# Kernel tuning notes

Hardware: AMD Instinct MI355X
Metric: run time of the kernel (lower is better)

Reference implementation:

```python
import jax, jax.numpy as jnp
import numpy as np

HEADS = 2
NEG_SLOPE = 0.2  # PyG GATConv default leaky_relu slope


def gat_conv(x, edge_index, W, a_src, a_dst, bias, num_nodes):
    """PyG-style GATConv with concat=True and self-loops.
    x: [N, Fin], W: [Fin, H*C], a_src/a_dst: [H, C], bias: [H*C].
    edge_index: [2, E] with row 0 = source j, row 1 = target i.
    """
    H = HEADS
    C = W.shape[1] // H
    # add self loops
    loops = jnp.arange(num_nodes, dtype=edge_index.dtype)
    src = jnp.concatenate([edge_index[0], loops])
    dst = jnp.concatenate([edge_index[1], loops])

    xW = (x @ W).reshape(num_nodes, H, C)            # [N, H, C]
    alpha_s = jnp.einsum('nhc,hc->nh', xW, a_src)    # [N, H]
    alpha_d = jnp.einsum('nhc,hc->nh', xW, a_dst)    # [N, H]
    e = alpha_s[src] + alpha_d[dst]                  # [E, H]
    e = jax.nn.leaky_relu(e, NEG_SLOPE)
    # segment softmax over edges sharing the same target node
    m = jax.ops.segment_max(e, dst, num_segments=num_nodes)  # [N, H]
    e = jnp.exp(e - m[dst])
    denom = jax.ops.segment_sum(e, dst, num_segments=num_nodes)  # [N, H]
    alpha = e / denom[dst]                           # [E, H]
    # message = alpha_ij * xW_j, aggregated at target i
    msg = xW[src] * alpha[:, :, None]                # [E, H, C]
    out = jax.ops.segment_sum(msg, dst, num_segments=num_nodes)  # [N, H, C]
    return out.reshape(num_nodes, H * C) + bias


def setup_inputs() -> dict:
    key = jax.random.key(0)
    ks = jax.random.split(key, 10)
    N, E = 50000, 800000
    Fin, D = 128, 128
    H = HEADS
    x = jax.random.normal(ks[0], (N, Fin), dtype=jnp.float32)
    edge_index = jax.random.randint(ks[1], (2, E), 0, N, dtype=jnp.int64)
    g = 1.0 / np.sqrt(Fin)
    W1 = jax.random.normal(ks[2], (Fin, H * D), dtype=jnp.float32) * g
    a_src1 = jax.random.normal(ks[3], (H, D), dtype=jnp.float32) * g
    a_dst1 = jax.random.normal(ks[4], (H, D), dtype=jnp.float32) * g
    b1 = jnp.zeros((H * D,), dtype=jnp.float32)
    g2 = 1.0 / np.sqrt(H * D)
    W2 = jax.random.normal(ks[5], (H * D, H * D), dtype=jnp.float32) * g2
    a_src2 = jax.random.normal(ks[6], (H, D), dtype=jnp.float32) * g2
    a_dst2 = jax.random.normal(ks[7], (H, D), dtype=jnp.float32) * g2
    b2 = jnp.zeros((H * D,), dtype=jnp.float32)
    return {"x": x, "edge_index": edge_index,
            "W1": W1, "a_src1": a_src1, "a_dst1": a_dst1, "b1": b1,
            "W2": W2, "a_src2": a_src2, "a_dst2": a_dst2, "b2": b2}


def reference(x, edge_index, W1, a_src1, a_dst1, b1, W2, a_src2, a_dst2, b2):
    N = x.shape[0]
    h = gat_conv(x, edge_index, W1, a_src1, a_dst1, b1, N)
    h = jax.nn.elu(h)
    # dropout is identity in eval mode (deterministic reference)
    out = gat_conv(h, edge_index, W2, a_src2, a_dst2, b2, N)
    return out
```

## Files before the change

### kernel.cpp

```cpp
#include <hip/hip_runtime.h>
#include <math.h>

#define HEADS 2
#define CH    128
#define HC    256
#define NEG   0.2f

typedef __attribute__((ext_vector_type(8))) short  bfrag8;
typedef __attribute__((ext_vector_type(4))) float  f32x4;

__device__ inline unsigned short f2bf_rne(float x) {
    unsigned u = __float_as_uint(x);
    u += 0x7fffu + ((u >> 16) & 1u);
    return (unsigned short)(u >> 16);
}

__global__ __launch_bounds__(256)
void wcast_kernel(const float* __restrict__ W, unsigned short* __restrict__ Wt, int K) {
    const int idx = blockIdx.x * 256 + threadIdx.x;
    if (idx >= K * HC) return;
    const int k = idx >> 8;
    const int n = idx & 255;
    Wt[(size_t)n * K + k] = f2bf_rne(W[idx]);
}

__global__ __launch_bounds__(256)
void va_kernel(const float* __restrict__ W, const float* __restrict__ a_src,
               const float* __restrict__ a_dst, float* __restrict__ va, int K) {
    const int k    = (blockIdx.x * 256 + threadIdx.x) >> 6;
    const int lane = threadIdx.x & 63;
    if (k >= K) return;
    const int c0 = lane * 4;
    const float4 w4 = *reinterpret_cast<const float4*>(&W[(size_t)k * HC + c0]);
    const float4 s4 = *reinterpret_cast<const float4*>(&a_src[c0]);
    const float4 d4 = *reinterpret_cast<const float4*>(&a_dst[c0]);
    float ps = w4.x * s4.x + w4.y * s4.y + w4.z * s4.z + w4.w * s4.w;
    float pd = w4.x * d4.x + w4.y * d4.y + w4.z * d4.z + w4.w * d4.w;
    #pragma unroll
    for (int m = 1; m <= 16; m <<= 1) {
        ps += __shfl_xor(ps, m);
        pd += __shfl_xor(pd, m);
    }
    if (lane == 0)  { va[k * 4 + 0] = ps; va[k * 4 + 2] = pd; }
    if (lane == 32) { va[k * 4 + 1] = ps; va[k * 4 + 3] = pd; }
}

__global__ __launch_bounds__(256)
void xprep_kernel(const float* __restrict__ x, const float* __restrict__ va,
                  unsigned short* __restrict__ xb, float* __restrict__ as_out,
                  float* __restrict__ ad_out, int N, int K) {
    const int i    = (blockIdx.x * 256 + threadIdx.x) >> 6;
    const int lane = threadIdx.x & 63;
    if (i >= N) return;
    const float2 v = reinterpret_cast<const float2*>(&x[(size_t)i * K])[lane];
    ushort2 bv; bv.x = f2bf_rne(v.x); bv.y = f2bf_rne(v.y);
    reinterpret_cast<ushort2*>(&xb[(size_t)i * K])[lane] = bv;

    const float4 a0 = reinterpret_cast<const float4*>(va)[lane * 2 + 0];
    const float4 a1 = reinterpret_cast<const float4*>(va)[lane * 2 + 1];
    float p0 = v.x * a0.x + v.y * a1.x;
    float p1 = v.x * a0.y + v.y * a1.y;
    float p2 = v.x * a0.z + v.y * a1.z;
    float p3 = v.x * a0.w + v.y * a1.w;
    #pragma unroll
    for (int m = 1; m <= 32; m <<= 1) {
        p0 += __shfl_xor(p0, m);
        p1 += __shfl_xor(p1, m);
        p2 += __shfl_xor(p2, m);
        p3 += __shfl_xor(p3, m);
    }
    if (lane == 0) {
        as_out[i * 2 + 0] = p0; as_out[i * 2 + 1] = p1;
        ad_out[i * 2 + 0] = p2; ad_out[i * 2 + 1] = p3;
    }
}

__global__ __launch_bounds__(256)
void gemm_msg_kernel(const unsigned short* __restrict__ Ab,
                     const unsigned short* __restrict__ Wt,
                     unsigned short* __restrict__ xWb, int M, int K) {
    __shared__ unsigned short Ah[128][40];
    __shared__ unsigned short Bh[128][40];

    const int t    = threadIdx.x;
    const int row0 = blockIdx.x * 128;
    const int col0 = blockIdx.y * 128;
    const int lane = t & 63;
    const int wid  = t >> 6;
    const int wr   = wid >> 1;
    const int wc   = wid & 1;

    f32x4 acc[4][4] = {};

    const int arow = t & 127;
    const int aseg = (t >> 7) * 16;

    for (int kk = 0; kk < K; kk += 32) {
        {
            const int gr = row0 + arow;
            bfrag8 v0 = {0,0,0,0,0,0,0,0}, v1 = {0,0,0,0,0,0,0,0};
            if (gr < M) {
                v0 = *reinterpret_cast<const bfrag8*>(&Ab[(size_t)gr * K + kk + aseg]);
                v1 = *reinterpret_cast<const bfrag8*>(&Ab[(size_t)gr * K + kk + aseg + 8]);
            }
            *reinterpret_cast<bfrag8*>(&Ah[arow][aseg])     = v0;
            *reinterpret_cast<bfrag8*>(&Ah[arow][aseg + 8]) = v1;
            const bfrag8 w0 = *reinterpret_cast<const bfrag8*>(
                &Wt[(size_t)(col0 + arow) * K + kk + aseg]);
            const bfrag8 w1 = *reinterpret_cast<const bfrag8*>(
                &Wt[(size_t)(col0 + arow) * K + kk + aseg + 8]);
            *reinterpret_cast<bfrag8*>(&Bh[arow][aseg])     = w0;
            *reinterpret_cast<bfrag8*>(&Bh[arow][aseg + 8]) = w1;
        }
        __syncthreads();

        bfrag8 ah[4], bh[4];
        const int ko = (lane >> 4) * 8;
        #pragma unroll
        for (int m = 0; m < 4; ++m)
            ah[m] = *reinterpret_cast<const bfrag8*>(&Ah[wr * 64 + m * 16 + (lane & 15)][ko]);
        #pragma unroll
        for (int n = 0; n < 4; ++n)
            bh[n] = *reinterpret_cast<const bfrag8*>(&Bh[wc * 64 + n * 16 + (lane & 15)][ko]);

        #pragma unroll
        for (int m = 0; m < 4; ++m)
            #pragma unroll
            for (int n = 0; n < 4; ++n)
                acc[m][n] = __builtin_amdgcn_mfma_f32_16x16x32_bf16(ah[m], bh[n], acc[m][n], 0, 0, 0);
        __syncthreads();
    }

    #pragma unroll
    for (int m = 0; m < 4; ++m) {
        #pragma unroll
        for (int reg = 0; reg < 4; ++reg) {
            const int gr = row0 + wr * 64 + m * 16 + (lane >> 4) * 4 + reg;
            if (gr < M) {
                unsigned short* rp = &xWb[(size_t)gr * HC + col0];
                #pragma unroll
                for (int n = 0; n < 4; ++n)
                    rp[wc * 64 + n * 16 + (lane & 15)] = f2bf_rne(acc[m][n][reg]);
            }
        }
    }
}

__global__ __launch_bounds__(256)
void hist_kernel(const int* __restrict__ dst, int* __restrict__ counts, int E) {
    const int e = blockIdx.x * 256 + threadIdx.x;
    if (e < E) atomicAdd(&counts[dst[e]], 1);
}

__global__ __launch_bounds__(256)
void scan_local_kernel(int* __restrict__ data, int* __restrict__ chunk_sum, int N) {
    __shared__ int s[256];
    const int t   = threadIdx.x;
    const int idx = blockIdx.x * 256 + t;
    const int v   = (idx < N) ? data[idx] : 0;
    s[t] = v;
    __syncthreads();
    #pragma unroll
    for (int off = 1; off < 256; off <<= 1) {
        int x = (t >= off) ? s[t - off] : 0;
        __syncthreads();
        s[t] += x;
        __syncthreads();
    }
    if (idx < N) data[idx] = s[t] - v;
    if (t == 255) chunk_sum[blockIdx.x] = s[255];
}

__global__ __launch_bounds__(256)
void scan_chunks_kernel(int* __restrict__ chunk, int nb) {
    __shared__ int s[256];
    const int t = threadIdx.x;
    const int v = (t < nb) ? chunk[t] : 0;
    s[t] = v;
    __syncthreads();
    #pragma unroll
    for (int off = 1; off < 256; off <<= 1) {
        int x = (t >= off) ? s[t - off] : 0;
        __syncthreads();
        s[t] += x;
        __syncthreads();
    }
    if (t < nb) chunk[t] = s[t] - v;
}

__global__ __launch_bounds__(256)
void add_offsets_kernel(const int* __restrict__ excl, const int* __restrict__ chunk_excl,
                        int* __restrict__ row_ptr, int* __restrict__ cursor,
                        int N, int E) {
    const int idx = blockIdx.x * 256 + threadIdx.x;
    if (idx < N) {
        const int rp = excl[idx] + chunk_excl[idx >> 8];
        row_ptr[idx] = rp;
        cursor[idx]  = rp;
    }
    if (idx == 0) row_ptr[N] = E;
}

__global__ __launch_bounds__(256)
void scatter_kernel(const int* __restrict__ src, const int* __restrict__ dst,
                    int* __restrict__ cursor, int* __restrict__ col_idx, int E) {
    const int e = blockIdx.x * 256 + threadIdx.x;
    if (e < E) {
        const int pos = atomicAdd(&cursor[dst[e]], 1);
        col_idx[pos] = src[e];
    }
}

__global__ __launch_bounds__(256)
void agg_kernel(const int* __restrict__ row_ptr, const int* __restrict__ col_idx,
                const unsigned short* __restrict__ xWb,
                const float* __restrict__ as_, const float* __restrict__ ad_,
                const float* __restrict__ bias, float* __restrict__ outf,
                unsigned short* __restrict__ hb, const float* __restrict__ va,
                float* __restrict__ as2, float* __restrict__ ad2,
                int N, int mode) {
    const int wv   = (blockIdx.x * 256 + threadIdx.x) >> 6;
    const int lane = threadIdx.x & 63;
    if (wv >= N) return;
    const int i    = wv;
    const int half = lane >> 5;
    const int sl   = lane & 31;
    const int hh   = sl >> 4;
    const int cb   = hh * 128 + (sl & 15) * 8;
    const float adi = ad_[i * 2 + hh];

    float acc[8] = {};
    float dn = 0.f;

    const int beg = row_ptr[i];
    const int end = row_ptr[i + 1];

    int k = beg + half;
    int j = (k < end) ? col_idx[k] : 0;
    float asj = as_[j * 2 + hh];
    for (; k < end; k += 2) {
        const int kn = k + 2;
        const int jn = (kn < end) ? col_idx[kn] : 0;
        const float asn = as_[jn * 2 + hh];
        float e = asj + adi;
        e = e > 0.f ? e : NEG * e;
        const float w = expf(e);
        const uint4 q = *reinterpret_cast<const uint4*>(&xWb[(size_t)j * HC + cb]);
        const unsigned qq[4] = {q.x, q.y, q.z, q.w};
        #pragma unroll
        for (int r = 0; r < 4; ++r) {
            const float flo = __uint_as_float(qq[r] << 16);
            const float fhi = __uint_as_float(qq[r] & 0xffff0000u);
            acc[r * 2 + 0] = fmaf(w, flo, acc[r * 2 + 0]);
            acc[r * 2 + 1] = fmaf(w, fhi, acc[r * 2 + 1]);
        }
        dn += w;
        j = jn; asj = asn;
    }

    #pragma unroll
    for (int r = 0; r < 8; ++r) acc[r] += __shfl_xor(acc[r], 32);
    dn += __shfl_xor(dn, 32);

    if (lane < 32) {
        float e = as_[i * 2 + hh] + adi;
        e = e > 0.f ? e : NEG * e;
        const float ws = expf(e);
        const uint4 q = *reinterpret_cast<const uint4*>(&xWb[(size_t)i * HC + cb]);
        const unsigned qq[4] = {q.x, q.y, q.z, q.w};
        #pragma unroll
        for (int r = 0; r < 4; ++r) {
            const float flo = __uint_as_float(qq[r] << 16);
            const float fhi = __uint_as_float(qq[r] & 0xffff0000u);
            acc[r * 2 + 0] = fmaf(ws, flo, acc[r * 2 + 0]);
            acc[r * 2 + 1] = fmaf(ws, fhi, acc[r * 2 + 1]);
        }
        dn += ws;

        const float inv = 1.f / dn;
        const float4 b0 = *reinterpret_cast<const float4*>(&bias[cb]);
        const float4 b1 = *reinterpret_cast<const float4*>(&bias[cb + 4]);
        float o[8];
        o[0] = acc[0] * inv + b0.x; o[1] = acc[1] * inv + b0.y;
        o[2] = acc[2] * inv + b0.z; o[3] = acc[3] * inv + b0.w;
        o[4] = acc[4] * inv + b1.x; o[5] = acc[5] * inv + b1.y;
        o[6] = acc[6] * inv + b1.z; o[7] = acc[7] * inv + b1.w;

        if (mode) {
            #pragma unroll
            for (int r = 0; r < 8; ++r) o[r] = o[r] > 0.f ? o[r] : expm1f(o[r]);
            bfrag8 hv;
            #pragma unroll
            for (int r = 0; r < 8; ++r) hv[r] = (short)f2bf_rne(o[r]);
            *reinterpret_cast<bfrag8*>(&hb[(size_t)i * HC + cb]) = hv;
            float p0 = 0.f, p1 = 0.f, p2 = 0.f, p3 = 0.f;
            #pragma unroll
            for (int r = 0; r < 8; ++r) {
                const float4 vv = reinterpret_cast<const float4*>(va)[cb + r];
                p0 = fmaf(o[r], vv.x, p0);
                p1 = fmaf(o[r], vv.y, p1);
                p2 = fmaf(o[r], vv.z, p2);
                p3 = fmaf(o[r], vv.w, p3);
            }
            #pragma unroll
            for (int m = 1; m <= 16; m <<= 1) {
                p0 += __shfl_xor(p0, m);
                p1 += __shfl_xor(p1, m);
                p2 += __shfl_xor(p2, m);
                p3 += __shfl_xor(p3, m);
            }
            if (sl == 0) {
                as2[i * 2 + 0] = p0; as2[i * 2 + 1] = p1;
                ad2[i * 2 + 0] = p2; ad2[i * 2 + 1] = p3;
            }
        } else {
            *reinterpret_cast<float4*>(&outf[(size_t)i * HC + cb]) =
                make_float4(o[0], o[1], o[2], o[3]);
            *reinterpret_cast<float4*>(&outf[(size_t)i * HC + cb + 4]) =
                make_float4(o[4], o[5], o[6], o[7]);
        }
    }
}

extern "C" void kernel_launch(void* const* d_in, const int* in_sizes, int n_in,
                              void* d_out, int out_size, void* d_ws, size_t ws_size,
                              hipStream_t stream) {
    const float* x      = (const float*)d_in[0];
    const int*   ei     = (const int*)d_in[1];
    const float* W1     = (const float*)d_in[2];
    const float* a_src1 = (const float*)d_in[3];
    const float* a_dst1 = (const float*)d_in[4];
    const float* b1     = (const float*)d_in[5];
    const float* W2     = (const float*)d_in[6];
    const float* a_src2 = (const float*)d_in[7];
    const float* a_dst2 = (const float*)d_in[8];
    const float* b2     = (const float*)d_in[9];
    float* out = (float*)d_out;

    const int Nn = in_sizes[0] / 128;
    const int E  = in_sizes[1] / 2;
    const int K1 = in_sizes[2] / HC;
    const int* src = ei;
    const int* dst = ei + E;

    float* as1   = (float*)d_ws;
    float* ad1   = as1 + (size_t)Nn * 2;
    float* as2   = ad1 + (size_t)Nn * 2;
    float* ad2   = as2 + (size_t)Nn * 2;
    float* va1   = ad2 + (size_t)Nn * 2;
    float* va2   = va1 + (size_t)K1 * 4;
    int*   tmp   = (int*)(va2 + (size_t)HC * 4);
    int*   chunk = tmp + Nn;
    int*   rowp  = chunk + 256;
    int*   curs  = rowp + (Nn + 1);
    int*   colx  = curs + Nn;
    uintptr_t pa = ((uintptr_t)(colx + E) + 31) & ~(uintptr_t)31;
    unsigned short* wt1 = (unsigned short*)pa;
    unsigned short* wt2 = wt1 + (size_t)HC * K1;
    unsigned short* xb  = wt2 + (size_t)HC * HC;
    unsigned short* xWb = xb  + (size_t)Nn * K1;
    unsigned short* hb  = xWb + (size_t)Nn * HC;

    const int nb = (Nn + 255) / 256;

    wcast_kernel<<<(K1 * HC + 255) / 256, 256, 0, stream>>>(W1, wt1, K1);
    wcast_kernel<<<(HC * HC + 255) / 256, 256, 0, stream>>>(W2, wt2, HC);
    va_kernel<<<(K1 + 3) / 4, 256, 0, stream>>>(W1, a_src1, a_dst1, va1, K1);
    va_kernel<<<(HC + 3) / 4, 256, 0, stream>>>(W2, a_src2, a_dst2, va2, HC);
    xprep_kernel<<<(Nn + 3) / 4, 256, 0, stream>>>(x, va1, xb, as1, ad1, Nn, K1);

    hipMemsetAsync(tmp, 0, (size_t)Nn * sizeof(int), stream);
    hist_kernel<<<(E + 255) / 256, 256, 0, stream>>>(dst, tmp, E);
    scan_local_kernel<<<nb, 256, 0, stream>>>(tmp, chunk, Nn);
    scan_chunks_kernel<<<1, 256, 0, stream>>>(chunk, nb);
    add_offsets_kernel<<<nb, 256, 0, stream>>>(tmp, chunk, rowp, curs, Nn, E);
    scatter_kernel<<<(E + 255) / 256, 256, 0, stream>>>(src, dst, curs, colx, E);

    const dim3 ggrid((Nn + 127) / 128, HC / 128);
    const int  agrid = (Nn + 3) / 4;

    gemm_msg_kernel<<<ggrid, 256, 0, stream>>>(xb, wt1, xWb, Nn, K1);
    agg_kernel<<<agrid, 256, 0, stream>>>(rowp, colx, xWb, as1, ad1, b1,
                                          (float*)nullptr, hb, va2, as2, ad2, Nn, 1);

    gemm_msg_kernel<<<ggrid, 256, 0, stream>>>(hb, wt2, xWb, Nn, HC);
    agg_kernel<<<agrid, 256, 0, stream>>>(rowp, colx, xWb, as2, ad2, b2,
                                          out, (unsigned short*)nullptr,
                                          (const float*)nullptr,
                                          (float*)nullptr, (float*)nullptr, Nn, 0);
}
```

Before: 335.5 us.

## Switch bf16 storage and MFMA to fp16, prefetch neighbor rows in aggregation

Changes all 16-bit intermediates (cast weights, inputs, xW, hidden) from bf16 to fp16 and uses the fp16 MFMA instruction instead of the bf16 one. In the aggregation loop it now prefetches the next neighbor's feature row together with its index, and uses the fast __expf. The intent is more accurate intermediates at the same bandwidth, a simpler unpack, and better hiding of gather latency. fp16 has a narrower range, so large values could overflow.

```diff
diff --git a/kernel.cpp b/kernel.cpp
--- a/kernel.cpp
+++ b/kernel.cpp
@@ -6,13 +6,14 @@
 #define HC    256
 #define NEG   0.2f
 
-typedef __attribute__((ext_vector_type(8))) short  bfrag8;
-typedef __attribute__((ext_vector_type(4))) float  f32x4;
-
-__device__ inline unsigned short f2bf_rne(float x) {
-    unsigned u = __float_as_uint(x);
-    u += 0x7fffu + ((u >> 16) & 1u);
-    return (unsigned short)(u >> 16);
+typedef __attribute__((ext_vector_type(8))) _Float16 half8;
+typedef __attribute__((ext_vector_type(4))) float    f32x4;
+
+__device__ inline unsigned short f2h(float x) {
+    _Float16 h = (_Float16)x;
+    unsigned short u;
+    __builtin_memcpy(&u, &h, 2);
+    return u;
 }
 
 __global__ __launch_bounds__(256)
@@ -21,7 +22,7 @@
     if (idx >= K * HC) return;
     const int k = idx >> 8;
     const int n = idx & 255;
-    Wt[(size_t)n * K + k] = f2bf_rne(W[idx]);
+    Wt[(size_t)n * K + k] = f2h(W[idx]);
 }
 
 __global__ __launch_bounds__(256)
@@ -53,7 +54,7 @@
     const int lane = threadIdx.x & 63;
     if (i >= N) return;
     const float2 v = reinterpret_cast<const float2*>(&x[(size_t)i * K])[lane];
-    ushort2 bv; bv.x = f2bf_rne(v.x); bv.y = f2bf_rne(v.y);
+    ushort2 bv; bv.x = f2h(v.x); bv.y = f2h(v.y);
     reinterpret_cast<ushort2*>(&xb[(size_t)i * K])[lane] = bv;
 
     const float4 a0 = reinterpret_cast<const float4*>(va)[lane * 2 + 0];
@@ -78,7 +79,7 @@
 __global__ __launch_bounds__(256)
 void gemm_msg_kernel(const unsigned short* __restrict__ Ab,
                      const unsigned short* __restrict__ Wt,
-                     unsigned short* __restrict__ xWb, int M, int K) {
+                     unsigned short* __restrict__ xWh, int M, int K) {
     __shared__ unsigned short Ah[128][40];
     __shared__ unsigned short Bh[128][40];
 
@@ -98,36 +99,36 @@
     for (int kk = 0; kk < K; kk += 32) {
         {
             const int gr = row0 + arow;
-            bfrag8 v0 = {0,0,0,0,0,0,0,0}, v1 = {0,0,0,0,0,0,0,0};
+            half8 v0 = {0,0,0,0,0,0,0,0}, v1 = {0,0,0,0,0,0,0,0};
             if (gr < M) {
-                v0 = *reinterpret_cast<const bfrag8*>(&Ab[(size_t)gr * K + kk + aseg]);
-                v1 = *reinterpret_cast<const bfrag8*>(&Ab[(size_t)gr * K + kk + aseg + 8]);
-            }
-            *reinterpret_cast<bfrag8*>(&Ah[arow][aseg])     = v0;
-            *reinterpret_cast<bfrag8*>(&Ah[arow][aseg + 8]) = v1;
-            const bfrag8 w0 = *reinterpret_cast<const bfrag8*>(
+                v0 = *reinterpret_cast<const half8*>(&Ab[(size_t)gr * K + kk + aseg]);
+                v1 = *reinterpret_cast<const half8*>(&Ab[(size_t)gr * K + kk + aseg + 8]);
+            }
+            *reinterpret_cast<half8*>(&Ah[arow][aseg])     = v0;
+            *reinterpret_cast<half8*>(&Ah[arow][aseg + 8]) = v1;
+            const half8 w0 = *reinterpret_cast<const half8*>(
                 &Wt[(size_t)(col0 + arow) * K + kk + aseg]);
-            const bfrag8 w1 = *reinterpret_cast<const bfrag8*>(
+            const half8 w1 = *reinterpret_cast<const half8*>(
                 &Wt[(size_t)(col0 + arow) * K + kk + aseg + 8]);
-            *reinterpret_cast<bfrag8*>(&Bh[arow][aseg])     = w0;
-            *reinterpret_cast<bfrag8*>(&Bh[arow][aseg + 8]) = w1;
+            *reinterpret_cast<half8*>(&Bh[arow][aseg])     = w0;
+            *reinterpret_cast<half8*>(&Bh[arow][aseg + 8]) = w1;
         }
         __syncthreads();
 
-        bfrag8 ah[4], bh[4];
+        half8 ah[4], bh[4];
         const int ko = (lane >> 4) * 8;
         #pragma unroll
         for (int m = 0; m < 4; ++m)
-            ah[m] = *reinterpret_cast<const bfrag8*>(&Ah[wr * 64 + m * 16 + (lane & 15)][ko]);
+            ah[m] = *reinterpret_cast<const half8*>(&Ah[wr * 64 + m * 16 + (lane & 15)][ko]);
         #pragma unroll
         for (int n = 0; n < 4; ++n)
-            bh[n] = *reinterpret_cast<const bfrag8*>(&Bh[wc * 64 + n * 16 + (lane & 15)][ko]);
+            bh[n] = *reinterpret_cast<const half8*>(&Bh[wc * 64 + n * 16 + (lane & 15)][ko]);
 
         #pragma unroll
         for (int m = 0; m < 4; ++m)
             #pragma unroll
             for (int n = 0; n < 4; ++n)
-                acc[m][n] = __builtin_amdgcn_mfma_f32_16x16x32_bf16(ah[m], bh[n], acc[m][n], 0, 0, 0);
+                acc[m][n] = __builtin_amdgcn_mfma_f32_16x16x32_f16(ah[m], bh[n], acc[m][n], 0, 0, 0);
         __syncthreads();
     }
 
@@ -137,10 +138,10 @@
         for (int reg = 0; reg < 4; ++reg) {
             const int gr = row0 + wr * 64 + m * 16 + (lane >> 4) * 4 + reg;
             if (gr < M) {
-                unsigned short* rp = &xWb[(size_t)gr * HC + col0];
+                unsigned short* rp = &xWh[(size_t)gr * HC + col0];
                 #pragma unroll
                 for (int n = 0; n < 4; ++n)
-                    rp[wc * 64 + n * 16 + (lane & 15)] = f2bf_rne(acc[m][n][reg]);
+                    rp[wc * 64 + n * 16 + (lane & 15)] = f2h(acc[m][n][reg]);
             }
         }
     }
@@ -213,7 +214,7 @@
 
 __global__ __launch_bounds__(256)
 void agg_kernel(const int* __restrict__ row_ptr, const int* __restrict__ col_idx,
-                const unsigned short* __restrict__ xWb,
+                const unsigned short* __restrict__ xWh,
                 const float* __restrict__ as_, const float* __restrict__ ad_,
                 const float* __restrict__ bias, float* __restrict__ outf,
                 unsigned short* __restrict__ hb, const float* __restrict__ va,
@@ -236,26 +237,31 @@
     const int end = row_ptr[i + 1];
 
     int k = beg + half;
-    int j = (k < end) ? col_idx[k] : 0;
-    float asj = as_[j * 2 + hh];
+    float asj = 0.f;
+    half8 hv = {0,0,0,0,0,0,0,0};
+    if (k < end) {
+        const int j0 = col_idx[k];
+        asj = as_[j0 * 2 + hh];
+        hv  = *reinterpret_cast<const half8*>(&xWh[(size_t)j0 * HC + cb]);
+    }
     for (; k < end; k += 2) {
         const int kn = k + 2;
-        const int jn = (kn < end) ? col_idx[kn] : 0;
-        const float asn = as_[jn * 2 + hh];
+        int jn = 0;
+        float asn = 0.f;
+        half8 hn = {0,0,0,0,0,0,0,0};
+        if (kn < end) {
+            jn  = col_idx[kn];
+            asn = as_[jn * 2 + hh];
+            hn  = *reinterpret_cast<const half8*>(&xWh[(size_t)jn * HC + cb]);
+        }
         float e = asj + adi;
         e = e > 0.f ? e : NEG * e;
-        const float w = expf(e);
-        const uint4 q = *reinterpret_cast<const uint4*>(&xWb[(size_t)j * HC + cb]);
-        const unsigned qq[4] = {q.x, q.y, q.z, q.w};
-        #pragma unroll
-        for (int r = 0; r < 4; ++r) {
-            const float flo = __uint_as_float(qq[r] << 16);
-            const float fhi = __uint_as_float(qq[r] & 0xffff0000u);
-            acc[r * 2 + 0] = fmaf(w, flo, acc[r * 2 + 0]);
-            acc[r * 2 + 1] = fmaf(w, fhi, acc[r * 2 + 1]);
-        }
+        const float w = __expf(e);
+        #pragma unroll
+        for (int r = 0; r < 8; ++r)
+            acc[r] = fmaf(w, (float)hv[r], acc[r]);
         dn += w;
-        j = jn; asj = asn;
+        hv = hn; asj = asn;
     }
 
     #pragma unroll
@@ -265,16 +271,11 @@
     if (lane < 32) {
         float e = as_[i * 2 + hh] + adi;
         e = e > 0.f ? e : NEG * e;
-        const float ws = expf(e);
-        const uint4 q = *reinterpret_cast<const uint4*>(&xWb[(size_t)i * HC + cb]);
-        const unsigned qq[4] = {q.x, q.y, q.z, q.w};
-        #pragma unroll
-        for (int r = 0; r < 4; ++r) {
-            const float flo = __uint_as_float(qq[r] << 16);
-            const float fhi = __uint_as_float(qq[r] & 0xffff0000u);
-            acc[r * 2 + 0] = fmaf(ws, flo, acc[r * 2 + 0]);
-            acc[r * 2 + 1] = fmaf(ws, fhi, acc[r * 2 + 1]);
-        }
+        const float ws = __expf(e);
+        const half8 sv = *reinterpret_cast<const half8*>(&xWh[(size_t)i * HC + cb]);
+        #pragma unroll
+        for (int r = 0; r < 8; ++r)
+            acc[r] = fmaf(ws, (float)sv[r], acc[r]);
         dn += ws;
 
         const float inv = 1.f / dn;
@@ -289,10 +290,10 @@
         if (mode) {
             #pragma unroll
             for (int r = 0; r < 8; ++r) o[r] = o[r] > 0.f ? o[r] : expm1f(o[r]);
-            bfrag8 hv;
-            #pragma unroll
-            for (int r = 0; r < 8; ++r) hv[r] = (short)f2bf_rne(o[r]);
-            *reinterpret_cast<bfrag8*>(&hb[(size_t)i * HC + cb]) = hv;
+            half8 hvo;
+            #pragma unroll
+            for (int r = 0; r < 8; ++r) hvo[r] = (_Float16)o[r];
+            *reinterpret_cast<half8*>(&hb[(size_t)i * HC + cb]) = hvo;
             float p0 = 0.f, p1 = 0.f, p2 = 0.f, p3 = 0.f;
             #pragma unroll
             for (int r = 0; r < 8; ++r) {
@@ -358,8 +359,8 @@
     unsigned short* wt1 = (unsigned short*)pa;
     unsigned short* wt2 = wt1 + (size_t)HC * K1;
     unsigned short* xb  = wt2 + (size_t)HC * HC;
-    unsigned short* xWb = xb  + (size_t)Nn * K1;
-    unsigned short* hb  = xWb + (size_t)Nn * HC;
+    unsigned short* xWh = xb  + (size_t)Nn * K1;
+    unsigned short* hb  = xWh + (size_t)Nn * HC;
 
     const int nb = (Nn + 255) / 256;
 
@@ -379,12 +380,12 @@
     const dim3 ggrid((Nn + 127) / 128, HC / 128);
     const int  agrid = (Nn + 3) / 4;
 
-    gemm_msg_kernel<<<ggrid, 256, 0, stream>>>(xb, wt1, xWb, Nn, K1);
-    agg_kernel<<<agrid, 256, 0, stream>>>(rowp, colx, xWb, as1, ad1, b1,
+    gemm_msg_kernel<<<ggrid, 256, 0, stream>>>(xb, wt1, xWh, Nn, K1);
+    agg_kernel<<<agrid, 256, 0, stream>>>(rowp, colx, xWh, as1, ad1, b1,
                                           (float*)nullptr, hb, va2, as2, ad2, Nn, 1);
 
-    gemm_msg_kernel<<<ggrid, 256, 0, stream>>>(hb, wt2, xWb, Nn, HC);
-    agg_kernel<<<agrid, 256, 0, stream>>>(rowp, colx, xWb, as2, ad2, b2,
+    gemm_msg_kernel<<<ggrid, 256, 0, stream>>>(hb, wt2, xWh, Nn, HC);
+    agg_kernel<<<agrid, 256, 0, stream>>>(rowp, colx, xWh, as2, ad2, b2,
                                           out, (unsigned short*)nullptr,
                                           (const float*)nullptr,
                                           (float*)nullptr, (float*)nullptr, Nn, 0);
```

After: 333.9 us. Within noise of the previous version (-0.5%).
